# Kernel optimization log

Hardware: AMD Instinct MI355X
Metric: run time of the kernel (lower is better)

Reference implementation:

```python
import jax, jax.numpy as jnp
import numpy as np

B, S, D, H = 2, 2048, 1024, 16
HD = D // H  # 64


def setup_inputs() -> dict:
    key = jax.random.key(0)
    ks = jax.random.split(key, 10)
    sc = 1.0 / np.sqrt(D)
    return {
        "decoder_hs": jax.random.normal(ks[0], (B, S, D), jnp.float32),
        "encoder_hs": jax.random.normal(ks[1], (B, S, D), jnp.float32),
        "Wq": jax.random.normal(ks[2], (D, D), jnp.float32) * sc,
        "bq": jax.random.normal(ks[3], (D,), jnp.float32) * 0.02,
        "Wk": jax.random.normal(ks[4], (D, D), jnp.float32) * sc,
        "bk": jax.random.normal(ks[5], (D,), jnp.float32) * 0.02,
        "Wv": jax.random.normal(ks[6], (D, D), jnp.float32) * sc,
        "bv": jax.random.normal(ks[7], (D,), jnp.float32) * 0.02,
        "Wp": jax.random.normal(ks[8], (D, D), jnp.float32) * sc,
        "bp": jax.random.normal(ks[9], (D,), jnp.float32) * 0.02,
    }


def reference(decoder_hs, encoder_hs, Wq, bq, Wk, bk, Wv, bv, Wp, bp):
    b, s, d = decoder_hs.shape
    # torch nn.Linear: y = x @ W.T + b, W is [out, in]
    q = decoder_hs @ Wq.T + bq
    k = encoder_hs @ Wk.T + bk
    v = encoder_hs @ Wv.T + bv
    # head split: [b, s, d] -> [b, h, s, hd]
    q = q.reshape(b, s, H, HD).transpose(0, 2, 1, 3)
    k = k.reshape(b, s, H, HD).transpose(0, 2, 1, 3)
    v = v.reshape(b, s, H, HD).transpose(0, 2, 1, 3)
    scale = 1.0 / np.sqrt(HD).astype(np.float32)
    att = jnp.einsum('bhqd,bhkd->bhqk', q, k) * scale
    att = jax.nn.softmax(att, axis=-1)
    y = jnp.einsum('bhqk,bhkd->bhqd', att, v)
    y = y.transpose(0, 2, 1, 3).reshape(b, s, d)
    return y @ Wp.T + bp
```

## Files before the change

kernel.cpp:

```cpp
#include <hip/hip_runtime.h>
#include <hip/hip_bf16.h>
#include <cstdint>
#include <cstddef>

#define BB 2
#define SS 2048
#define DD 1024
#define HH 16
#define HD 64

typedef __attribute__((ext_vector_type(8))) short bf16x8;
typedef __attribute__((ext_vector_type(4))) short bf16x4;
typedef __attribute__((ext_vector_type(4))) float f32x4;

#define MFMA16(va, vb, c) __builtin_amdgcn_mfma_f32_16x16x16bf16_1k(va, vb, c, 0, 0, 0)

#define GLL(g, l) __builtin_amdgcn_global_load_lds( \
    (const __attribute__((address_space(1))) void*)(g), \
    (__attribute__((address_space(3))) void*)(l), 16, 0, 0)

__device__ __forceinline__ short f2bf_fast(float f) {
    uint32_t u = __float_as_uint(f);
    u += 0x7FFF + ((u >> 16) & 1);
    return (short)(u >> 16);
}
__device__ __forceinline__ uint32_t pack_bf2(float a, float b) {
    uint32_t ua = __float_as_uint(a), ub = __float_as_uint(b);
    ua += 0x7FFF + ((ua >> 16) & 1);
    ub += 0x7FFF + ((ub >> 16) & 1);
    return (ua >> 16) | (ub & 0xFFFF0000u);
}
__device__ __forceinline__ uint32_t cvtpk_bf2(float a, float b) {
    uint32_t r;
    asm("v_cvt_pk_bf16_f32 %0, %1, %2" : "=v"(r) : "v"(a), "v"(b));
    return r;
}
__device__ __forceinline__ bf16x8 cvt8(const float* __restrict__ p) {
    float4 a = *(const float4*)p;
    float4 b = *(const float4*)(p + 4);
    union { uint32_t d[4]; bf16x8 v; } r;
    r.d[0] = pack_bf2(a.x, a.y);
    r.d[1] = pack_bf2(a.z, a.w);
    r.d[2] = pack_bf2(b.x, b.y);
    r.d[3] = pack_bf2(b.z, b.w);
    return r.v;
}

__global__ __launch_bounds__(256) void cvt6_kernel(
    const float* __restrict__ s0, const float* __restrict__ s1,
    const float* __restrict__ s2, const float* __restrict__ s3,
    const float* __restrict__ s4, const float* __restrict__ s5,
    short* __restrict__ d0, short* __restrict__ d1, short* __restrict__ d2,
    short* __restrict__ d3, short* __restrict__ d4, short* __restrict__ d5)
{
    const int z = blockIdx.z;
    const float* s = (z == 0) ? s0 : (z == 1) ? s1 : (z == 2) ? s2
                   : (z == 3) ? s3 : (z == 4) ? s4 : s5;
    short* d = (z == 0) ? d0 : (z == 1) ? d1 : (z == 2) ? d2
             : (z == 3) ? d3 : (z == 4) ? d4 : d5;
    const int n8 = (z < 2) ? (BB * SS * DD / 8) : (DD * DD / 8);
    const int id = blockIdx.x * 256 + threadIdx.x;
    if (id >= n8) return;
    bf16x8 r = cvt8(s + (size_t)id * 8);
    *(uint4*)(d + (size_t)id * 8) = *(uint4*)&r;
}

template<int BF>
__global__ __launch_bounds__(256, 3) void qkv_gemm_kernel(
    const void* __restrict__ dec, const void* __restrict__ enc,
    const void* __restrict__ Wq, const void* __restrict__ Wk,
    const void* __restrict__ Wv,
    const float* __restrict__ bq, const float* __restrict__ bk,
    const float* __restrict__ bv,
    short* __restrict__ Qo, short* __restrict__ Ko, short* __restrict__ Vo)
{
    __shared__ short As[128 * 32];
    __shared__ short Bs[128 * 32];

    const int z = blockIdx.z;
    const void* Xv = (z == 0) ? dec : enc;
    const void* Wp_ = (z == 0) ? Wq : (z == 1) ? Wk : Wv;
    const float* bias = (z == 0) ? bq : (z == 1) ? bk : bv;
    short* Yo = (z == 0) ? Qo : (z == 1) ? Ko : Vo;
    const float qs = (z == 0) ? (0.125f * 1.44269504088896f) : 1.0f;

    const int t = threadIdx.x;
    const int lane = t & 63, wv = t >> 6;
    const int lr = lane & 15, quad = lane >> 4;
    const int wm = wv >> 1, wn = wv & 1;
    const int m0 = blockIdx.y * 128;
    const int n0 = blockIdx.x * 128;
    const int K = DD;

    f32x4 acc[4][4];
    #pragma unroll
    for (int i = 0; i < 4; i++)
        #pragma unroll
        for (int j = 0; j < 4; j++) acc[i][j] = (f32x4){0.f, 0.f, 0.f, 0.f};

    for (int kb = 0; kb < K; kb += 32) {
        __syncthreads();
        if (BF) {
            const short* Xb = (const short*)Xv;
            const short* Wb = (const short*)Wp_;
            #pragma unroll
            for (int c = 0; c < 2; c++) {
                int r0 = wv * 32 + c * 16;
                int r = r0 + (lane >> 2), ch = (lane & 3) * 8;
                GLL(Xb + (size_t)(m0 + r) * K + kb + ch, &As[r0 * 32]);
                GLL(Wb + (size_t)(n0 + r) * K + kb + ch, &Bs[r0 * 32]);
            }
        } else {
            const float* Xf = (const float*)Xv;
            const float* Wf = (const float*)Wp_;
            #pragma unroll
            for (int c = 0; c < 2; c++) {
                int id = t + c * 256;
                int r = id >> 2, c8 = (id & 3) * 8;
                *(bf16x8*)&As[r * 32 + c8] = cvt8(Xf + (size_t)(m0 + r) * K + kb + c8);
                *(bf16x8*)&Bs[r * 32 + c8] = cvt8(Wf + (size_t)(n0 + r) * K + kb + c8);
            }
        }
        __syncthreads();

        bf16x8 af[4], bfr[4];
        #pragma unroll
        for (int mi = 0; mi < 4; mi++)
            af[mi] = *(const bf16x8*)&As[(wm * 64 + mi * 16 + lr) * 32 + quad * 8];
        #pragma unroll
        for (int ni = 0; ni < 4; ni++)
            bfr[ni] = *(const bf16x8*)&Bs[(wn * 64 + ni * 16 + lr) * 32 + quad * 8];
        #pragma unroll
        for (int mi = 0; mi < 4; mi++)
            #pragma unroll
            for (int ni = 0; ni < 4; ni++)
                acc[mi][ni] = __builtin_amdgcn_mfma_f32_16x16x32_bf16(
                    af[mi], bfr[ni], acc[mi][ni], 0, 0, 0);
    }

    if (z < 2) {
        #pragma unroll
        for (int ni = 0; ni < 4; ni++) {
            int col = n0 + wn * 64 + ni * 16 + lr;
            int h = col >> 6, hd = col & 63;
            float bvv = bias[col];
            #pragma unroll
            for (int mi = 0; mi < 4; mi++) {
                #pragma unroll
                for (int r2 = 0; r2 < 4; r2++) {
                    int row = m0 + wm * 64 + mi * 16 + quad * 4 + r2;
                    int b = row >> 11, s = row & 2047;
                    float v = (acc[mi][ni][r2] + bvv) * qs;
                    size_t off = ((size_t)(b * HH + h) * SS + s) * HD + hd;
                    Yo[off] = f2bf_fast(v);
                }
            }
        }
    } else {
        #pragma unroll
        for (int ni = 0; ni < 4; ni++) {
            int col = n0 + wn * 64 + ni * 16 + lr;
            int h = col >> 6, hd = col & 63;
            float bvv = bias[col];
            #pragma unroll
            for (int mi = 0; mi < 4; mi++) {
                int s0 = m0 + wm * 64 + mi * 16 + quad * 4;
                int b = s0 >> 11, s = s0 & 2047;
                union { uint32_t d[2]; } u;
                u.d[0] = pack_bf2(acc[mi][ni][0] + bvv, acc[mi][ni][1] + bvv);
                u.d[1] = pack_bf2(acc[mi][ni][2] + bvv, acc[mi][ni][3] + bvv);
                size_t off = ((size_t)(b * HH + h) * HD + hd) * SS + s;
                *(uint2*)(Yo + off) = *(uint2*)&u;
            }
        }
    }
}

template<int WBF>
__global__ __launch_bounds__(256, 2) void proj_gemm_kernel(
    const short* __restrict__ X,
    const void* __restrict__ W, const float* __restrict__ bias,
    float* __restrict__ Y)
{
    __shared__ short As[64 * 32];
    __shared__ short Bs[128 * 32];

    const int t = threadIdx.x;
    const int lane = t & 63, wv = t >> 6;
    const int lr = lane & 15, quad = lane >> 4;
    const int wm = wv >> 1, wn = wv & 1;
    const int m0 = blockIdx.y * 64;
    const int n0 = blockIdx.x * 128;
    const int K = DD, N = DD;

    f32x4 acc[2][4];
    #pragma unroll
    for (int i = 0; i < 2; i++)
        #pragma unroll
        for (int j = 0; j < 4; j++) acc[i][j] = (f32x4){0.f, 0.f, 0.f, 0.f};

    for (int kb = 0; kb < K; kb += 32) {
        __syncthreads();
        {
            int r0 = wv * 16;
            int r = r0 + (lane >> 2), ch = (lane & 3) * 8;
            GLL(X + (size_t)(m0 + r) * K + kb + ch, &As[r0 * 32]);
        }
        if (WBF) {
            const short* Wb = (const short*)W;
            #pragma unroll
            for (int c = 0; c < 2; c++) {
                int r0 = wv * 32 + c * 16;
                int r = r0 + (lane >> 2), ch = (lane & 3) * 8;
                GLL(Wb + (size_t)(n0 + r) * K + kb + ch, &Bs[r0 * 32]);
            }
        } else {
            const float* Wf = (const float*)W;
            #pragma unroll
            for (int c = 0; c < 2; c++) {
                int id = t + c * 256;
                int r = id >> 2, c8 = (id & 3) * 8;
                *(bf16x8*)&Bs[r * 32 + c8] = cvt8(Wf + (size_t)(n0 + r) * K + kb + c8);
            }
        }
        __syncthreads();

        bf16x8 af[2], bfr[4];
        #pragma unroll
        for (int mi = 0; mi < 2; mi++)
            af[mi] = *(const bf16x8*)&As[(wm * 32 + mi * 16 + lr) * 32 + quad * 8];
        #pragma unroll
        for (int ni = 0; ni < 4; ni++)
            bfr[ni] = *(const bf16x8*)&Bs[(wn * 64 + ni * 16 + lr) * 32 + quad * 8];
        #pragma unroll
        for (int mi = 0; mi < 2; mi++)
            #pragma unroll
            for (int ni = 0; ni < 4; ni++)
                acc[mi][ni] = __builtin_amdgcn_mfma_f32_16x16x32_bf16(
                    af[mi], bfr[ni], acc[mi][ni], 0, 0, 0);
    }

    #pragma unroll
    for (int ni = 0; ni < 4; ni++) {
        int col = n0 + wn * 64 + ni * 16 + lr;
        float bvv = bias[col];
        #pragma unroll
        for (int mi = 0; mi < 2; mi++) {
            #pragma unroll
            for (int r2 = 0; r2 < 4; r2++) {
                int row = m0 + wm * 32 + mi * 16 + quad * 4 + r2;
                Y[(size_t)row * N + col] = acc[mi][ni][r2] + bvv;
            }
        }
    }
}

__global__ __launch_bounds__(256, 2) void attn_kernel(
    const short* __restrict__ Q,
    const short* __restrict__ Kgl,
    const short* __restrict__ Vt_g,
    short* __restrict__ Y)
{
    __shared__ short Ks[2][128][64];
    __shared__ short Vt[2][64][128];

    const int t = threadIdx.x;
    const int lane = t & 63, w = t >> 6;
    const int lr = lane & 15, quad = lane >> 4;
    const int e = lr & 7;

    const int bid = blockIdx.x;
    const int slot = bid >> 3;
    const int bh = ((slot >> 4) << 3) + (bid & 7);
    const int qt = slot & 15;
    const int b = bh >> 4, h = bh & 15;

    const short* QpA = Q + ((size_t)bh * SS + qt * 128 + w * 32 + lr) * HD;
    const short* QpB = QpA + 16 * HD;
    bf16x8 qfA0 = *(const bf16x8*)(QpA + quad * 8);
    bf16x8 qfA1 = *(const bf16x8*)(QpA + 32 + quad * 8);
    bf16x8 qfB0 = *(const bf16x8*)(QpB + quad * 8);
    bf16x8 qfB1 = *(const bf16x8*)(QpB + 32 + quad * 8);

    f32x4 oA[4], oB[4];
    #pragma unroll
    for (int i = 0; i < 4; i++) {
        oA[i] = (f32x4){0.f, 0.f, 0.f, 0.f};
        oB[i] = (f32x4){0.f, 0.f, 0.f, 0.f};
    }
    f32x4 vsumA = (f32x4){0.f, 0.f, 0.f, 0.f};
    f32x4 vsumB = (f32x4){0.f, 0.f, 0.f, 0.f};

    const short* Kb = Kgl + (size_t)bh * SS * HD;
    const short* Vb = Vt_g + (size_t)bh * HD * SS;

    auto stage = [&](int kt1, int nb) {
        #pragma unroll
        for (int c = 0; c < 4; c++) {
            int r0 = w * 32 + c * 8;
            int r  = r0 + (lane >> 3);
            int sc = ((lane & 7) ^ (r & 7)) * 8;
            GLL(Kb + (size_t)(kt1 * 128 + r) * 64 + sc, &Ks[nb][r0][0]);
        }
        #pragma unroll
        for (int c = 0; c < 4; c++) {
            int h0 = w * 16 + c * 4;
            int hd = h0 + (lane >> 4);
            int s16 = (lane & 15) ^ (hd & 7);
            GLL(Vb + (size_t)hd * SS + kt1 * 128 + s16 * 8, &Vt[nb][h0][0]);
        }
    };

    stage(0, 0);
    __syncthreads();

    int cur = 0;
    for (int kt = 0; kt < SS / 128; kt++) {
        if (kt + 1 < SS / 128) stage(kt + 1, cur ^ 1);

        f32x4 scA[8], scB[8];
        __builtin_amdgcn_s_setprio(1);
        #pragma unroll
        for (int nt = 0; nt < 8; nt++) {
            const short* krow = &Ks[cur][nt * 16 + lr][0];
            bf16x8 kf0 = *(const bf16x8*)&krow[(quad ^ e) * 8];
            bf16x8 kf1 = *(const bf16x8*)&krow[((quad + 4) ^ e) * 8];
            scA[nt] = __builtin_amdgcn_mfma_f32_16x16x32_bf16(
                kf0, qfA0, (f32x4){0.f, 0.f, 0.f, 0.f}, 0, 0, 0);
            scA[nt] = __builtin_amdgcn_mfma_f32_16x16x32_bf16(kf1, qfA1, scA[nt], 0, 0, 0);
            scB[nt] = __builtin_amdgcn_mfma_f32_16x16x32_bf16(
                kf0, qfB0, (f32x4){0.f, 0.f, 0.f, 0.f}, 0, 0, 0);
            scB[nt] = __builtin_amdgcn_mfma_f32_16x16x32_bf16(kf1, qfB1, scB[nt], 0, 0, 0);
        }
        __builtin_amdgcn_s_setprio(0);

        bf16x4 pbA[8], pbB[8];
        #pragma unroll
        for (int nt = 0; nt < 8; nt++) {
            f32x4 ea, eb;
            ea[0] = __builtin_amdgcn_exp2f(scA[nt][0]);
            ea[1] = __builtin_amdgcn_exp2f(scA[nt][1]);
            ea[2] = __builtin_amdgcn_exp2f(scA[nt][2]);
            ea[3] = __builtin_amdgcn_exp2f(scA[nt][3]);
            vsumA += ea;
            union { uint32_t d[2]; bf16x4 v; } ua;
            ua.d[0] = cvtpk_bf2(ea[0], ea[1]);
            ua.d[1] = cvtpk_bf2(ea[2], ea[3]);
            pbA[nt] = ua.v;
            eb[0] = __builtin_amdgcn_exp2f(scB[nt][0]);
            eb[1] = __builtin_amdgcn_exp2f(scB[nt][1]);
            eb[2] = __builtin_amdgcn_exp2f(scB[nt][2]);
            eb[3] = __builtin_amdgcn_exp2f(scB[nt][3]);
            vsumB += eb;
            union { uint32_t d[2]; bf16x4 v; } ub;
            ub.d[0] = cvtpk_bf2(eb[0], eb[1]);
            ub.d[1] = cvtpk_bf2(eb[2], eb[3]);
            pbB[nt] = ub.v;
        }

        __builtin_amdgcn_s_setprio(1);
        #pragma unroll
        for (int dt = 0; dt < 4; dt++) {
            const short* vrow = &Vt[cur][dt * 16 + lr][0];
            #pragma unroll
            for (int nt = 0; nt < 8; nt++) {
                int ch = (nt * 2 + (quad >> 1)) ^ e;
                bf16x4 va = *(const bf16x4*)&vrow[ch * 8 + (quad & 1) * 4];
                oA[dt] = MFMA16(va, pbA[nt], oA[dt]);
                oB[dt] = MFMA16(va, pbB[nt], oB[dt]);
            }
        }
        __builtin_amdgcn_s_setprio(0);

        __syncthreads();
        cur ^= 1;
    }

    float lsumA = (vsumA[0] + vsumA[1]) + (vsumA[2] + vsumA[3]);
    float lsumB = (vsumB[0] + vsumB[1]) + (vsumB[2] + vsumB[3]);
    lsumA += __shfl_xor(lsumA, 16, 64);
    lsumA += __shfl_xor(lsumA, 32, 64);
    lsumB += __shfl_xor(lsumB, 16, 64);
    lsumB += __shfl_xor(lsumB, 32, 64);
    float invA = 1.0f / lsumA, invB = 1.0f / lsumB;

    const int srowA = qt * 128 + w * 32 + lr;
    short* YpA = Y + ((size_t)b * SS + srowA) * DD + h * 64 + quad * 4;
    short* YpB = YpA + 16 * DD;
    #pragma unroll
    for (int dt = 0; dt < 4; dt++) {
        union { uint32_t d[2]; } ua;
        ua.d[0] = pack_bf2(oA[dt][0] * invA, oA[dt][1] * invA);
        ua.d[1] = pack_bf2(oA[dt][2] * invA, oA[dt][3] * invA);
        *(uint2*)(YpA + dt * 16) = *(uint2*)&ua;
        union { uint32_t d[2]; } ub;
        ub.d[0] = pack_bf2(oB[dt][0] * invB, oB[dt][1] * invB);
        ub.d[1] = pack_bf2(oB[dt][2] * invB, oB[dt][3] * invB);
        *(uint2*)(YpB + dt * 16) = *(uint2*)&ub;
    }
}

extern "C" void kernel_launch(void* const* d_in, const int* in_sizes, int n_in,
                              void* d_out, int out_size, void* d_ws, size_t ws_size,
                              hipStream_t stream) {
    const float* dec = (const float*)d_in[0];
    const float* enc = (const float*)d_in[1];
    const float* Wq  = (const float*)d_in[2];
    const float* bq  = (const float*)d_in[3];
    const float* Wk  = (const float*)d_in[4];
    const float* bk  = (const float*)d_in[5];
    const float* Wv  = (const float*)d_in[6];
    const float* bv  = (const float*)d_in[7];
    const float* Wp  = (const float*)d_in[8];
    const float* bp  = (const float*)d_in[9];

    const size_t per = (size_t)BB * HH * SS * HD;
    const size_t wsz = (size_t)DD * DD;
    short* ws = (short*)d_ws;
    short* Qb  = ws;
    short* Kb  = ws + per;
    short* Vtb = ws + 2 * per;
    short* Yb  = ws + 3 * per;

    dim3 qkv_grid(DD / 128, (BB * SS) / 128, 3);
    dim3 proj_grid(DD / 128, (BB * SS) / 64);
    const int attn_blocks = BB * HH * (SS / 128);

    const size_t need = (6 * per + 4 * wsz) * sizeof(short);
    if (ws_size >= need) {
        short* decb = ws + 4 * per;
        short* encb = ws + 5 * per;
        short* Wqb  = ws + 6 * per;
        short* Wkb  = Wqb + wsz;
        short* Wvb  = Wqb + 2 * wsz;
        short* Wpb  = Wqb + 3 * wsz;
        cvt6_kernel<<<dim3((BB * SS * DD / 8 + 255) / 256, 1, 6), 256, 0, stream>>>(
            dec, enc, Wq, Wk, Wv, Wp, decb, encb, Wqb, Wkb, Wvb, Wpb);
        qkv_gemm_kernel<1><<<qkv_grid, 256, 0, stream>>>(
            decb, encb, Wqb, Wkb, Wvb, bq, bk, bv, Qb, Kb, Vtb);
        attn_kernel<<<attn_blocks, 256, 0, stream>>>(Qb, Kb, Vtb, Yb);
        proj_gemm_kernel<1><<<proj_grid, 256, 0, stream>>>(Yb, Wpb, bp, (float*)d_out);
    } else {
        qkv_gemm_kernel<0><<<qkv_grid, 256, 0, stream>>>(
            dec, enc, Wq, Wk, Wv, bq, bk, bv, Qb, Kb, Vtb);
        attn_kernel<<<attn_blocks, 256, 0, stream>>>(Qb, Kb, Vtb, Yb);
        proj_gemm_kernel<0><<<proj_grid, 256, 0, stream>>>(Yb, Wp, bp, (float*)d_out);
    }
}
```

Baseline: 204.2 us.

## Double-buffer LDS tiles in QKV and projection GEMMs; flatten conversion grid

The bf16 paths of the QKV and output-projection GEMMs now use two LDS buffers per operand. The next K-tile's global_load_lds is issued before the MFMAs on the current tile, with one barrier per iteration instead of two, so load latency can hide behind compute. The conversion kernel switches from a 3D grid with many idle z-slices to a flat grid covering exactly the element count, which removes wasted blocks. Doubling LDS per block may reduce occupancy, and correctness depends on the single barrier ordering async LDS writes against reads of the other buffer.

Result: no change. 207.5 us (+1.6%).

```diff
diff --git a/kernel.cpp b/kernel.cpp
--- a/kernel.cpp
+++ b/kernel.cpp
@@ -53,16 +53,21 @@
     short* __restrict__ d0, short* __restrict__ d1, short* __restrict__ d2,
     short* __restrict__ d3, short* __restrict__ d4, short* __restrict__ d5)
 {
-    const int z = blockIdx.z;
-    const float* s = (z == 0) ? s0 : (z == 1) ? s1 : (z == 2) ? s2
-                   : (z == 3) ? s3 : (z == 4) ? s4 : s5;
-    short* d = (z == 0) ? d0 : (z == 1) ? d1 : (z == 2) ? d2
-             : (z == 3) ? d3 : (z == 4) ? d4 : d5;
-    const int n8 = (z < 2) ? (BB * SS * DD / 8) : (DD * DD / 8);
     const int id = blockIdx.x * 256 + threadIdx.x;
-    if (id >= n8) return;
-    bf16x8 r = cvt8(s + (size_t)id * 8);
-    *(uint4*)(d + (size_t)id * 8) = *(uint4*)&r;
+    const float* s; short* d; size_t off;
+    if (id < 1048576) {
+        int e = id >> 19;
+        off = (size_t)(id & 524287) * 8;
+        s = e ? s1 : s0;  d = e ? d1 : d0;
+    } else {
+        int j = id - 1048576;
+        int w = j >> 17;
+        off = (size_t)(j & 131071) * 8;
+        s = (w == 0) ? s2 : (w == 1) ? s3 : (w == 2) ? s4 : s5;
+        d = (w == 0) ? d2 : (w == 1) ? d3 : (w == 2) ? d4 : d5;
+    }
+    bf16x8 r = cvt8(s + off);
+    *(uint4*)(d + off) = *(uint4*)&r;
 }
 
 template<int BF>
@@ -74,8 +79,8 @@
     const float* __restrict__ bv,
     short* __restrict__ Qo, short* __restrict__ Ko, short* __restrict__ Vo)
 {
-    __shared__ short As[128 * 32];
-    __shared__ short Bs[128 * 32];
+    __shared__ short As[2][128 * 32];
+    __shared__ short Bs[2][128 * 32];
 
     const int z = blockIdx.z;
     const void* Xv = (z == 0) ? dec : enc;
@@ -98,44 +103,69 @@
         #pragma unroll
         for (int j = 0; j < 4; j++) acc[i][j] = (f32x4){0.f, 0.f, 0.f, 0.f};
 
-    for (int kb = 0; kb < K; kb += 32) {
-        __syncthreads();
-        if (BF) {
-            const short* Xb = (const short*)Xv;
-            const short* Wb = (const short*)Wp_;
+    if (BF) {
+        const short* Xb = (const short*)Xv;
+        const short* Wb = (const short*)Wp_;
+        auto stage = [&](int kb, int nb) {
             #pragma unroll
             for (int c = 0; c < 2; c++) {
                 int r0 = wv * 32 + c * 16;
                 int r = r0 + (lane >> 2), ch = (lane & 3) * 8;
-                GLL(Xb + (size_t)(m0 + r) * K + kb + ch, &As[r0 * 32]);
-                GLL(Wb + (size_t)(n0 + r) * K + kb + ch, &Bs[r0 * 32]);
-            }
-        } else {
-            const float* Xf = (const float*)Xv;
-            const float* Wf = (const float*)Wp_;
+                GLL(Xb + (size_t)(m0 + r) * K + kb + ch, &As[nb][r0 * 32]);
+                GLL(Wb + (size_t)(n0 + r) * K + kb + ch, &Bs[nb][r0 * 32]);
+            }
+        };
+        stage(0, 0);
+        __syncthreads();
+        int cur = 0;
+        for (int kb = 0; kb < K; kb += 32) {
+            if (kb + 32 < K) stage(kb + 32, cur ^ 1);
+
+            bf16x8 af[4], bfr[4];
+            #pragma unroll
+            for (int mi = 0; mi < 4; mi++)
+                af[mi] = *(const bf16x8*)&As[cur][(wm * 64 + mi * 16 + lr) * 32 + quad * 8];
+            #pragma unroll
+            for (int ni = 0; ni < 4; ni++)
+                bfr[ni] = *(const bf16x8*)&Bs[cur][(wn * 64 + ni * 16 + lr) * 32 + quad * 8];
+            #pragma unroll
+            for (int mi = 0; mi < 4; mi++)
+                #pragma unroll
+                for (int ni = 0; ni < 4; ni++)
+                    acc[mi][ni] = __builtin_amdgcn_mfma_f32_16x16x32_bf16(
+                        af[mi], bfr[ni], acc[mi][ni], 0, 0, 0);
+
+            __syncthreads();
+            cur ^= 1;
+        }
+    } else {
+        const float* Xf = (const float*)Xv;
+        const float* Wf = (const float*)Wp_;
+        for (int kb = 0; kb < K; kb += 32) {
+            __syncthreads();
             #pragma unroll
             for (int c = 0; c < 2; c++) {
                 int id = t + c * 256;
                 int r = id >> 2, c8 = (id & 3) * 8;
-                *(bf16x8*)&As[r * 32 + c8] = cvt8(Xf + (size_t)(m0 + r) * K + kb + c8);
-                *(bf16x8*)&Bs[r * 32 + c8] = cvt8(Wf + (size_t)(n0 + r) * K + kb + c8);
-            }
-        }
-        __syncthreads();
-
-        bf16x8 af[4], bfr[4];
-        #pragma unroll
-        for (int mi = 0; mi < 4; mi++)
-            af[mi] = *(const bf16x8*)&As[(wm * 64 + mi * 16 + lr) * 32 + quad * 8];
-        #pragma unroll
-        for (int ni = 0; ni < 4; ni++)
-            bfr[ni] = *(const bf16x8*)&Bs[(wn * 64 + ni * 16 + lr) * 32 + quad * 8];
-        #pragma unroll
-        for (int mi = 0; mi < 4; mi++)
+                *(bf16x8*)&As[0][r * 32 + c8] = cvt8(Xf + (size_t)(m0 + r) * K + kb + c8);
+                *(bf16x8*)&Bs[0][r * 32 + c8] = cvt8(Wf + (size_t)(n0 + r) * K + kb + c8);
+            }
+            __syncthreads();
+
+            bf16x8 af[4], bfr[4];
+            #pragma unroll
+            for (int mi = 0; mi < 4; mi++)
+                af[mi] = *(const bf16x8*)&As[0][(wm * 64 + mi * 16 + lr) * 32 + quad * 8];
             #pragma unroll
             for (int ni = 0; ni < 4; ni++)
-                acc[mi][ni] = __builtin_amdgcn_mfma_f32_16x16x32_bf16(
-                    af[mi], bfr[ni], acc[mi][ni], 0, 0, 0);
+                bfr[ni] = *(const bf16x8*)&Bs[0][(wn * 64 + ni * 16 + lr) * 32 + quad * 8];
+            #pragma unroll
+            for (int mi = 0; mi < 4; mi++)
+                #pragma unroll
+                for (int ni = 0; ni < 4; ni++)
+                    acc[mi][ni] = __builtin_amdgcn_mfma_f32_16x16x32_bf16(
+                        af[mi], bfr[ni], acc[mi][ni], 0, 0, 0);
+        }
     }
 
     if (z < 2) {
@@ -182,8 +212,8 @@
     const void* __restrict__ W, const float* __restrict__ bias,
     float* __restrict__ Y)
 {
-    __shared__ short As[64 * 32];
-    __shared__ short Bs[128 * 32];
+    __shared__ short As[2][64 * 32];
+    __shared__ short Bs[2][128 * 32];
 
     const int t = threadIdx.x;
     const int lane = t & 63, wv = t >> 6;
@@ -199,45 +229,75 @@
         #pragma unroll
         for (int j = 0; j < 4; j++) acc[i][j] = (f32x4){0.f, 0.f, 0.f, 0.f};
 
-    for (int kb = 0; kb < K; kb += 32) {
-        __syncthreads();
-        {
-            int r0 = wv * 16;
-            int r = r0 + (lane >> 2), ch = (lane & 3) * 8;
-            GLL(X + (size_t)(m0 + r) * K + kb + ch, &As[r0 * 32]);
-        }
-        if (WBF) {
-            const short* Wb = (const short*)W;
+    if (WBF) {
+        const short* Wb = (const short*)W;
+        auto stage = [&](int kb, int nb) {
+            {
+                int r0 = wv * 16;
+                int r = r0 + (lane >> 2), ch = (lane & 3) * 8;
+                GLL(X + (size_t)(m0 + r) * K + kb + ch, &As[nb][r0 * 32]);
+            }
             #pragma unroll
             for (int c = 0; c < 2; c++) {
                 int r0 = wv * 32 + c * 16;
                 int r = r0 + (lane >> 2), ch = (lane & 3) * 8;
-                GLL(Wb + (size_t)(n0 + r) * K + kb + ch, &Bs[r0 * 32]);
-            }
-        } else {
-            const float* Wf = (const float*)W;
+                GLL(Wb + (size_t)(n0 + r) * K + kb + ch, &Bs[nb][r0 * 32]);
+            }
+        };
+        stage(0, 0);
+        __syncthreads();
+        int cur = 0;
+        for (int kb = 0; kb < K; kb += 32) {
+            if (kb + 32 < K) stage(kb + 32, cur ^ 1);
+
+            bf16x8 af[2], bfr[4];
+            #pragma unroll
+            for (int mi = 0; mi < 2; mi++)
+                af[mi] = *(const bf16x8*)&As[cur][(wm * 32 + mi * 16 + lr) * 32 + quad * 8];
+            #pragma unroll
+            for (int ni = 0; ni < 4; ni++)
+                bfr[ni] = *(const bf16x8*)&Bs[cur][(wn * 64 + ni * 16 + lr) * 32 + quad * 8];
+            #pragma unroll
+            for (int mi = 0; mi < 2; mi++)
+                #pragma unroll
+                for (int ni = 0; ni < 4; ni++)
+                    acc[mi][ni] = __builtin_amdgcn_mfma_f32_16x16x32_bf16(
+                        af[mi], bfr[ni], acc[mi][ni], 0, 0, 0);
+
+            __syncthreads();
+            cur ^= 1;
+        }
+    } else {
+        const float* Wf = (const float*)W;
+        for (int kb = 0; kb < K; kb += 32) {
+            __syncthreads();
+            {
+                int r0 = wv * 16;
+                int r = r0 + (lane >> 2), ch = (lane & 3) * 8;
+                GLL(X + (size_t)(m0 + r) * K + kb + ch, &As[0][r0 * 32]);
+            }
             #pragma unroll
             for (int c = 0; c < 2; c++) {
                 int id = t + c * 256;
                 int r = id >> 2, c8 = (id & 3) * 8;
-                *(bf16x8*)&Bs[r * 32 + c8] = cvt8(Wf + (size_t)(n0 + r) * K + kb + c8);
-            }
-        }
-        __syncthreads();
-
-        bf16x8 af[2], bfr[4];
-        #pragma unroll
-        for (int mi = 0; mi < 2; mi++)
-            af[mi] = *(const bf16x8*)&As[(wm * 32 + mi * 16 + lr) * 32 + quad * 8];
-        #pragma unroll
-        for (int ni = 0; ni < 4; ni++)
-            bfr[ni] = *(const bf16x8*)&Bs[(wn * 64 + ni * 16 + lr) * 32 + quad * 8];
-        #pragma unroll
-        for (int mi = 0; mi < 2; mi++)
+                *(bf16x8*)&Bs[0][r * 32 + c8] = cvt8(Wf + (size_t)(n0 + r) * K + kb + c8);
+            }
+            __syncthreads();
+
+            bf16x8 af[2], bfr[4];
+            #pragma unroll
+            for (int mi = 0; mi < 2; mi++)
+                af[mi] = *(const bf16x8*)&As[0][(wm * 32 + mi * 16 + lr) * 32 + quad * 8];
             #pragma unroll
             for (int ni = 0; ni < 4; ni++)
-                acc[mi][ni] = __builtin_amdgcn_mfma_f32_16x16x32_bf16(
-                    af[mi], bfr[ni], acc[mi][ni], 0, 0, 0);
+                bfr[ni] = *(const bf16x8*)&Bs[0][(wn * 64 + ni * 16 + lr) * 32 + quad * 8];
+            #pragma unroll
+            for (int mi = 0; mi < 2; mi++)
+                #pragma unroll
+                for (int ni = 0; ni < 4; ni++)
+                    acc[mi][ni] = __builtin_amdgcn_mfma_f32_16x16x32_bf16(
+                        af[mi], bfr[ni], acc[mi][ni], 0, 0, 0);
+        }
     }
 
     #pragma unroll
@@ -425,6 +485,7 @@
     dim3 qkv_grid(DD / 128, (BB * SS) / 128, 3);
     dim3 proj_grid(DD / 128, (BB * SS) / 64);
     const int attn_blocks = BB * HH * (SS / 128);
+    const int cvt_blocks = (2 * 524288 + 4 * 131072) / 256;
 
     const size_t need = (6 * per + 4 * wsz) * sizeof(short);
     if (ws_size >= need) {
@@ -434,7 +495,7 @@
         short* Wkb  = Wqb + wsz;
         short* Wvb  = Wqb + 2 * wsz;
         short* Wpb  = Wqb + 3 * wsz;
-        cvt6_kernel<<<dim3((BB * SS * DD / 8 + 255) / 256, 1, 6), 256, 0, stream>>>(
+        cvt6_kernel<<<cvt_blocks, 256, 0, stream>>>(
             dec, enc, Wq, Wk, Wv, Wp, decb, encb, Wqb, Wkb, Wvb, Wpb);
         qkv_gemm_kernel<1><<<qkv_grid, 256, 0, stream>>>(
             decb, encb, Wqb, Wkb, Wvb, bq, bk, bv, Qb, Kb, Vtb);
```

## Switch attention to 32x32x16 MFMA with permlane32 swap for P operand

Applied to the files above, without the earlier changes.

The attention kernel now has each wave own 32 query rows in a single 32x32 MFMA tile instead of two 16x16 tiles. It computes QK^T and PV with the 32x32x16 bf16 instruction and rearranges the exponentiated scores into B-operand layout using v_permlane32_swap. This cuts the number of MFMA issues and LDS fragment loads per tile and removes one shuffle step from the row-sum reduction. Separately, the conversion kernel uses a flat grid sized exactly to the work instead of a 6-slice z-grid, which previously launched many idle blocks for the weight slices.

After: 203.4 us. Within noise of the previous version (-0.4%).

```diff
diff --git a/kernel.cpp b/kernel.cpp
--- a/kernel.cpp
+++ b/kernel.cpp
@@ -10,10 +10,8 @@
 #define HD 64
 
 typedef __attribute__((ext_vector_type(8))) short bf16x8;
-typedef __attribute__((ext_vector_type(4))) short bf16x4;
 typedef __attribute__((ext_vector_type(4))) float f32x4;
-
-#define MFMA16(va, vb, c) __builtin_amdgcn_mfma_f32_16x16x16bf16_1k(va, vb, c, 0, 0, 0)
+typedef __attribute__((ext_vector_type(16))) float f32x16;
 
 #define GLL(g, l) __builtin_amdgcn_global_load_lds( \
     (const __attribute__((address_space(1))) void*)(g), \
@@ -34,6 +32,9 @@
     uint32_t r;
     asm("v_cvt_pk_bf16_f32 %0, %1, %2" : "=v"(r) : "v"(a), "v"(b));
     return r;
+}
+__device__ __forceinline__ void pl32swap(uint32_t& a, uint32_t& b) {
+    asm("v_permlane32_swap_b32 %0, %1" : "+v"(a), "+v"(b));
 }
 __device__ __forceinline__ bf16x8 cvt8(const float* __restrict__ p) {
     float4 a = *(const float4*)p;
@@ -53,16 +54,21 @@
     short* __restrict__ d0, short* __restrict__ d1, short* __restrict__ d2,
     short* __restrict__ d3, short* __restrict__ d4, short* __restrict__ d5)
 {
-    const int z = blockIdx.z;
-    const float* s = (z == 0) ? s0 : (z == 1) ? s1 : (z == 2) ? s2
-                   : (z == 3) ? s3 : (z == 4) ? s4 : s5;
-    short* d = (z == 0) ? d0 : (z == 1) ? d1 : (z == 2) ? d2
-             : (z == 3) ? d3 : (z == 4) ? d4 : d5;
-    const int n8 = (z < 2) ? (BB * SS * DD / 8) : (DD * DD / 8);
     const int id = blockIdx.x * 256 + threadIdx.x;
-    if (id >= n8) return;
-    bf16x8 r = cvt8(s + (size_t)id * 8);
-    *(uint4*)(d + (size_t)id * 8) = *(uint4*)&r;
+    const float* s; short* d; size_t off;
+    if (id < 1048576) {
+        int e = id >> 19;
+        off = (size_t)(id & 524287) * 8;
+        s = e ? s1 : s0;  d = e ? d1 : d0;
+    } else {
+        int j = id - 1048576;
+        int w = j >> 17;
+        off = (size_t)(j & 131071) * 8;
+        s = (w == 0) ? s2 : (w == 1) ? s3 : (w == 2) ? s4 : s5;
+        d = (w == 0) ? d2 : (w == 1) ? d3 : (w == 2) ? d4 : d5;
+    }
+    bf16x8 r = cvt8(s + off);
+    *(uint4*)(d + off) = *(uint4*)&r;
 }
 
 template<int BF>
@@ -266,8 +272,8 @@
 
     const int t = threadIdx.x;
     const int lane = t & 63, w = t >> 6;
-    const int lr = lane & 15, quad = lane >> 4;
-    const int e = lr & 7;
+    const int lq = lane & 31, hf = lane >> 5;
+    const int e = lq & 7;
 
     const int bid = blockIdx.x;
     const int slot = bid >> 3;
@@ -275,21 +281,17 @@
     const int qt = slot & 15;
     const int b = bh >> 4, h = bh & 15;
 
-    const short* QpA = Q + ((size_t)bh * SS + qt * 128 + w * 32 + lr) * HD;
-    const short* QpB = QpA + 16 * HD;
-    bf16x8 qfA0 = *(const bf16x8*)(QpA + quad * 8);
-    bf16x8 qfA1 = *(const bf16x8*)(QpA + 32 + quad * 8);
-    bf16x8 qfB0 = *(const bf16x8*)(QpB + quad * 8);
-    bf16x8 qfB1 = *(const bf16x8*)(QpB + 32 + quad * 8);
-
-    f32x4 oA[4], oB[4];
-    #pragma unroll
-    for (int i = 0; i < 4; i++) {
-        oA[i] = (f32x4){0.f, 0.f, 0.f, 0.f};
-        oB[i] = (f32x4){0.f, 0.f, 0.f, 0.f};
-    }
-    f32x4 vsumA = (f32x4){0.f, 0.f, 0.f, 0.f};
-    f32x4 vsumB = (f32x4){0.f, 0.f, 0.f, 0.f};
+    const int q = qt * 128 + w * 32 + lq;
+    const short* Qp = Q + ((size_t)bh * SS + q) * HD;
+    bf16x8 qf[4];
+    #pragma unroll
+    for (int j = 0; j < 4; j++)
+        qf[j] = *(const bf16x8*)(Qp + j * 16 + hf * 8);
+
+    f32x16 o[2];
+    #pragma unroll
+    for (int i = 0; i < 16; i++) { o[0][i] = 0.f; o[1][i] = 0.f; }
+    f32x4 vsum = (f32x4){0.f, 0.f, 0.f, 0.f};
 
     const short* Kb = Kgl + (size_t)bh * SS * HD;
     const short* Vb = Vt_g + (size_t)bh * HD * SS;
@@ -318,57 +320,49 @@
     for (int kt = 0; kt < SS / 128; kt++) {
         if (kt + 1 < SS / 128) stage(kt + 1, cur ^ 1);
 
-        f32x4 scA[8], scB[8];
+        bf16x8 pb[4][2];
+        #pragma unroll
+        for (int s = 0; s < 4; s++) {
+            const short* krow = &Ks[cur][s * 32 + lq][0];
+            f32x16 sc = (f32x16){0.f,0.f,0.f,0.f,0.f,0.f,0.f,0.f,
+                                 0.f,0.f,0.f,0.f,0.f,0.f,0.f,0.f};
+            __builtin_amdgcn_s_setprio(1);
+            #pragma unroll
+            for (int j = 0; j < 4; j++) {
+                bf16x8 kf = *(const bf16x8*)&krow[((j * 2 + hf) ^ e) * 8];
+                sc = __builtin_amdgcn_mfma_f32_32x32x16_bf16(kf, qf[j], sc, 0, 0, 0);
+            }
+            __builtin_amdgcn_s_setprio(0);
+
+            float ev[16];
+            #pragma unroll
+            for (int i = 0; i < 16; i++) ev[i] = __builtin_amdgcn_exp2f(sc[i]);
+            #pragma unroll
+            for (int r = 0; r < 4; r++)
+                vsum += (f32x4){ev[4*r], ev[4*r+1], ev[4*r+2], ev[4*r+3]};
+            uint32_t dw[8];
+            #pragma unroll
+            for (int i = 0; i < 8; i++) dw[i] = cvtpk_bf2(ev[2*i], ev[2*i+1]);
+            pl32swap(dw[0], dw[2]); pl32swap(dw[1], dw[3]);
+            pl32swap(dw[4], dw[6]); pl32swap(dw[5], dw[7]);
+            union { uint32_t u[4]; bf16x8 v; } f0, f1;
+            f0.u[0] = dw[0]; f0.u[1] = dw[1]; f0.u[2] = dw[2]; f0.u[3] = dw[3];
+            f1.u[0] = dw[4]; f1.u[1] = dw[5]; f1.u[2] = dw[6]; f1.u[3] = dw[7];
+            pb[s][0] = f0.v; pb[s][1] = f1.v;
+        }
+
         __builtin_amdgcn_s_setprio(1);
         #pragma unroll
-        for (int nt = 0; nt < 8; nt++) {
-            const short* krow = &Ks[cur][nt * 16 + lr][0];
-            bf16x8 kf0 = *(const bf16x8*)&krow[(quad ^ e) * 8];
-            bf16x8 kf1 = *(const bf16x8*)&krow[((quad + 4) ^ e) * 8];
-            scA[nt] = __builtin_amdgcn_mfma_f32_16x16x32_bf16(
-                kf0, qfA0, (f32x4){0.f, 0.f, 0.f, 0.f}, 0, 0, 0);
-            scA[nt] = __builtin_amdgcn_mfma_f32_16x16x32_bf16(kf1, qfA1, scA[nt], 0, 0, 0);
-            scB[nt] = __builtin_amdgcn_mfma_f32_16x16x32_bf16(
-                kf0, qfB0, (f32x4){0.f, 0.f, 0.f, 0.f}, 0, 0, 0);
-            scB[nt] = __builtin_amdgcn_mfma_f32_16x16x32_bf16(kf1, qfB1, scB[nt], 0, 0, 0);
-        }
-        __builtin_amdgcn_s_setprio(0);
-
-        bf16x4 pbA[8], pbB[8];
-        #pragma unroll
-        for (int nt = 0; nt < 8; nt++) {
-            f32x4 ea, eb;
-            ea[0] = __builtin_amdgcn_exp2f(scA[nt][0]);
-            ea[1] = __builtin_amdgcn_exp2f(scA[nt][1]);
-            ea[2] = __builtin_amdgcn_exp2f(scA[nt][2]);
-            ea[3] = __builtin_amdgcn_exp2f(scA[nt][3]);
-            vsumA += ea;
-            union { uint32_t d[2]; bf16x4 v; } ua;
-            ua.d[0] = cvtpk_bf2(ea[0], ea[1]);
-            ua.d[1] = cvtpk_bf2(ea[2], ea[3]);
-            pbA[nt] = ua.v;
-            eb[0] = __builtin_amdgcn_exp2f(scB[nt][0]);
-            eb[1] = __builtin_amdgcn_exp2f(scB[nt][1]);
-            eb[2] = __builtin_amdgcn_exp2f(scB[nt][2]);
-            eb[3] = __builtin_amdgcn_exp2f(scB[nt][3]);
-            vsumB += eb;
-            union { uint32_t d[2]; bf16x4 v; } ub;
-            ub.d[0] = cvtpk_bf2(eb[0], eb[1]);
-            ub.d[1] = cvtpk_bf2(eb[2], eb[3]);
-            pbB[nt] = ub.v;
-        }
-
-        __builtin_amdgcn_s_setprio(1);
-        #pragma unroll
-        for (int dt = 0; dt < 4; dt++) {
-            const short* vrow = &Vt[cur][dt * 16 + lr][0];
-            #pragma unroll
-            for (int nt = 0; nt < 8; nt++) {
-                int ch = (nt * 2 + (quad >> 1)) ^ e;
-                bf16x4 va = *(const bf16x4*)&vrow[ch * 8 + (quad & 1) * 4];
-                oA[dt] = MFMA16(va, pbA[nt], oA[dt]);
-                oB[dt] = MFMA16(va, pbB[nt], oB[dt]);
-            }
+        for (int ds = 0; ds < 2; ds++) {
+            const short* vrow = &Vt[cur][ds * 32 + lq][0];
+            #pragma unroll
+            for (int s = 0; s < 4; s++)
+                #pragma unroll
+                for (int c = 0; c < 2; c++) {
+                    bf16x8 va = *(const bf16x8*)&vrow[((s * 4 + c * 2 + hf) ^ e) * 8];
+                    o[ds] = __builtin_amdgcn_mfma_f32_32x32x16_bf16(
+                        va, pb[s][c], o[ds], 0, 0, 0);
+                }
         }
         __builtin_amdgcn_s_setprio(0);
 
@@ -376,28 +370,20 @@
         cur ^= 1;
     }
 
-    float lsumA = (vsumA[0] + vsumA[1]) + (vsumA[2] + vsumA[3]);
-    float lsumB = (vsumB[0] + vsumB[1]) + (vsumB[2] + vsumB[3]);
-    lsumA += __shfl_xor(lsumA, 16, 64);
-    lsumA += __shfl_xor(lsumA, 32, 64);
-    lsumB += __shfl_xor(lsumB, 16, 64);
-    lsumB += __shfl_xor(lsumB, 32, 64);
-    float invA = 1.0f / lsumA, invB = 1.0f / lsumB;
-
-    const int srowA = qt * 128 + w * 32 + lr;
-    short* YpA = Y + ((size_t)b * SS + srowA) * DD + h * 64 + quad * 4;
-    short* YpB = YpA + 16 * DD;
-    #pragma unroll
-    for (int dt = 0; dt < 4; dt++) {
-        union { uint32_t d[2]; } ua;
-        ua.d[0] = pack_bf2(oA[dt][0] * invA, oA[dt][1] * invA);
-        ua.d[1] = pack_bf2(oA[dt][2] * invA, oA[dt][3] * invA);
-        *(uint2*)(YpA + dt * 16) = *(uint2*)&ua;
-        union { uint32_t d[2]; } ub;
-        ub.d[0] = pack_bf2(oB[dt][0] * invB, oB[dt][1] * invB);
-        ub.d[1] = pack_bf2(oB[dt][2] * invB, oB[dt][3] * invB);
-        *(uint2*)(YpB + dt * 16) = *(uint2*)&ub;
-    }
+    float lsum = (vsum[0] + vsum[1]) + (vsum[2] + vsum[3]);
+    lsum += __shfl_xor(lsum, 32, 64);
+    float inv = 1.0f / lsum;
+
+    short* Yp = Y + ((size_t)b * SS + q) * DD + h * 64 + hf * 4;
+    #pragma unroll
+    for (int ds = 0; ds < 2; ds++)
+        #pragma unroll
+        for (int rr = 0; rr < 4; rr++) {
+            union { uint32_t d[2]; } u;
+            u.d[0] = pack_bf2(o[ds][rr*4+0] * inv, o[ds][rr*4+1] * inv);
+            u.d[1] = pack_bf2(o[ds][rr*4+2] * inv, o[ds][rr*4+3] * inv);
+            *(uint2*)(Yp + ds * 32 + rr * 8) = *(uint2*)&u;
+        }
 }
 
 extern "C" void kernel_launch(void* const* d_in, const int* in_sizes, int n_in,
@@ -425,6 +411,7 @@
     dim3 qkv_grid(DD / 128, (BB * SS) / 128, 3);
     dim3 proj_grid(DD / 128, (BB * SS) / 64);
     const int attn_blocks = BB * HH * (SS / 128);
+    const int cvt_blocks = (2 * 524288 + 4 * 131072) / 256;
 
     const size_t need = (6 * per + 4 * wsz) * sizeof(short);
     if (ws_size >= need) {
@@ -434,7 +421,7 @@
         short* Wkb  = Wqb + wsz;
         short* Wvb  = Wqb + 2 * wsz;
         short* Wpb  = Wqb + 3 * wsz;
-        cvt6_kernel<<<dim3((BB * SS * DD / 8 + 255) / 256, 1, 6), 256, 0, stream>>>(
+        cvt6_kernel<<<cvt_blocks, 256, 0, stream>>>(
             dec, enc, Wq, Wk, Wv, Wp, decb, encb, Wqb, Wkb, Wvb, Wpb);
         qkv_gemm_kernel<1><<<qkv_grid, 256, 0, stream>>>(
             decb, encb, Wqb, Wkb, Wvb, bq, bk, bv, Qb, Kb, Vtb);
```
